# Kernel tuning notes

Measured on AMD Instinct MI355X. Metric: run time of the kernel, lower is better.

## Reference

```python
import jax, jax.numpy as jnp
import numpy as np

CODEBOOK_SIZE = 4096
DIM = 64


def setup_inputs() -> dict:
    key = jax.random.key(0)
    kx, ke = jax.random.split(key)
    x = jax.random.normal(kx, (8, 4096, DIM), dtype=jnp.float32)
    embed = jax.random.normal(ke, (CODEBOOK_SIZE, DIM), dtype=jnp.float32)  # codebook [K, d]
    return {"x": x, "embed": embed}


def reference(x, embed):
    # Eval-mode forward of EuclideanCodebook (svq_temp=None -> argmax).
    shape = x.shape
    flatten = x.reshape(-1, shape[-1])            # [N, d]
    embed_sq = jnp.sum(embed * embed, axis=-1)    # [K]
    # dist = 2 * x @ embed.T - ||embed||^2  (negative squared distance up to a const in x)
    dist = 2.0 * jnp.matmul(flatten, embed.T) - embed_sq[None, :]  # [N, K]
    embed_ind = jnp.argmax(dist, axis=-1)         # [N]
    embed_ind = embed_ind.reshape(shape[:-1])     # [...]
    quantize = embed[embed_ind]                   # gather -> [..., d]
    return (quantize, embed_ind)
```

## Files before the change

kernel.cpp:

```cpp
#include <hip/hip_runtime.h>
#include <math.h>

#define N_ROWS 32768
#define K_CODES 4096
#define DIM 64
#define SPLITS 4
#define TILES_TOTAL (K_CODES / 32)
#define TILES_PER_SPLIT (TILES_TOTAL / SPLITS)
#define QUANT_ELEMS (N_ROWS * DIM)

typedef _Float16 half8 __attribute__((ext_vector_type(8)));
typedef float floatx16 __attribute__((ext_vector_type(16)));

__device__ __forceinline__ void gld16(const void* g, void* l) {
    __builtin_amdgcn_global_load_lds(
        (const __attribute__((address_space(1))) unsigned int*)g,
        (__attribute__((address_space(3))) unsigned int*)l, 16, 0, 0);
}

__global__ void prep_kernel(const float* __restrict__ embed,
                            float* __restrict__ sq, half8* __restrict__ ehi,
                            half8* __restrict__ elo) {
    __shared__ float part[256];
    const int tid = threadIdx.x;
    const int t = blockIdx.x * 256 + tid;
    const int l = t & 63;
    const int s = (t >> 6) & 3;
    const int c = blockIdx.x;
    const int col = l & 31;
    const int code = c * 32 + col;
    const int koff = (l >> 5) * 8 + 16 * s;
    const float* src = embed + (size_t)code * DIM + koff;
    half8 h, lo;
    float ss = 0.f;
#pragma unroll
    for (int j = 0; j < 8; ++j) {
        float v = src[j];
        ss = fmaf(v, v, ss);
        _Float16 hi = (_Float16)v;
        h[j] = hi;
        lo[j] = (_Float16)(v - (float)hi);
    }
    ehi[t] = h;
    elo[t] = lo;
    part[tid] = ss;
    __syncthreads();
    if (tid < 32) {
        float a = 0.f;
#pragma unroll
        for (int q = 0; q < 8; ++q) a += part[tid + 32 * (q & 1) + 64 * (q >> 1)];
        sq[c * 32 + tid] = a;
    }
}

__global__ __launch_bounds__(256, 4) void fused_dist_argmax32(
    const float* __restrict__ x, const float* __restrict__ sq,
    const half8* __restrict__ ehi, const half8* __restrict__ elo,
    float* __restrict__ pbest, int* __restrict__ pidx) {
    __shared__ char lbuf[8192];
    const int tid = threadIdx.x;
    const int lane = tid & 63;
    const int wave = tid >> 6;
    const int col = lane & 31;
    const int half_ = lane >> 5;
    const int row_base = blockIdx.x * 128 + wave * 32;
    const int split = blockIdx.y;
    const int c0 = split * TILES_PER_SPLIT;

    half8 ah[4], al[4];
    {
        const float* xs = x + (size_t)(row_base + col) * DIM + half_ * 8;
#pragma unroll
        for (int s = 0; s < 4; ++s) {
            half8 h, lo;
#pragma unroll
            for (int j = 0; j < 8; ++j) {
                float v = 2.0f * xs[16 * s + j];
                _Float16 hi = (_Float16)v;
                h[j] = hi;
                lo[j] = (_Float16)(v - (float)hi);
            }
            ah[s] = h;
            al[s] = lo;
        }
    }

    float best[16];
    int bidx[16];
#pragma unroll
    for (int r = 0; r < 16; ++r) {
        best[r] = -INFINITY;
        bidx[r] = 0;
    }

    const char* gh = (const char*)(ehi + (size_t)c0 * 256);
    const char* gl = (const char*)(elo + (size_t)c0 * 256);
    const float* psq = sq + c0 * 32 + col;
    const half8* lh = (const half8*)lbuf;
    const half8* ll = (const half8*)(lbuf + 4096);

    for (int c = 0; c < TILES_PER_SPLIT; ++c) {
        gld16(gh + (size_t)c * 4096 + (size_t)tid * 16, lbuf + tid * 16);
        gld16(gl + (size_t)c * 4096 + (size_t)tid * 16, lbuf + 4096 + tid * 16);
        float nsq = -psq[(size_t)c * 32];
        __syncthreads();

        floatx16 acc;
#pragma unroll
        for (int r = 0; r < 16; ++r) acc[r] = nsq;
        half8 b;
        b = lh[lane];
        acc = __builtin_amdgcn_mfma_f32_32x32x16_f16(ah[0], b, acc, 0, 0, 0);
        acc = __builtin_amdgcn_mfma_f32_32x32x16_f16(al[0], b, acc, 0, 0, 0);
        b = lh[64 + lane];
        acc = __builtin_amdgcn_mfma_f32_32x32x16_f16(ah[1], b, acc, 0, 0, 0);
        acc = __builtin_amdgcn_mfma_f32_32x32x16_f16(al[1], b, acc, 0, 0, 0);
        b = lh[128 + lane];
        acc = __builtin_amdgcn_mfma_f32_32x32x16_f16(ah[2], b, acc, 0, 0, 0);
        acc = __builtin_amdgcn_mfma_f32_32x32x16_f16(al[2], b, acc, 0, 0, 0);
        b = lh[192 + lane];
        acc = __builtin_amdgcn_mfma_f32_32x32x16_f16(ah[3], b, acc, 0, 0, 0);
        acc = __builtin_amdgcn_mfma_f32_32x32x16_f16(al[3], b, acc, 0, 0, 0);
        b = ll[lane];
        acc = __builtin_amdgcn_mfma_f32_32x32x16_f16(ah[0], b, acc, 0, 0, 0);
        b = ll[64 + lane];
        acc = __builtin_amdgcn_mfma_f32_32x32x16_f16(ah[1], b, acc, 0, 0, 0);
        b = ll[128 + lane];
        acc = __builtin_amdgcn_mfma_f32_32x32x16_f16(ah[2], b, acc, 0, 0, 0);
        b = ll[192 + lane];
        acc = __builtin_amdgcn_mfma_f32_32x32x16_f16(ah[3], b, acc, 0, 0, 0);
        __syncthreads();

        const int cidx = (c0 + c) * 32 + col;
#pragma unroll
        for (int r = 0; r < 16; ++r) {
            if (acc[r] > best[r]) {
                best[r] = acc[r];
                bidx[r] = cidx;
            }
        }
    }

#pragma unroll
    for (int r = 0; r < 16; ++r) {
        float bv = best[r];
        int bi = bidx[r];
#pragma unroll
        for (int d = 1; d < 32; d <<= 1) {
            float ov = __shfl_xor(bv, d);
            int oi = __shfl_xor(bi, d);
            if (ov > bv || (ov == bv && oi < bi)) {
                bv = ov;
                bi = oi;
            }
        }
        if (col == 0) {
            const int row = row_base + (r & 3) + 8 * (r >> 2) + 4 * half_;
            pbest[(size_t)split * N_ROWS + row] = bv;
            pidx[(size_t)split * N_ROWS + row] = bi;
        }
    }
}

__global__ void combine_kernel(const float* __restrict__ pbest,
                               const int* __restrict__ pidx,
                               const float* __restrict__ embed,
                               float* __restrict__ out) {
    const int t = blockIdx.x * blockDim.x + threadIdx.x;
    const int row = t >> 4;
    const int q = t & 15;
    if (row >= N_ROWS) return;

    float best = -INFINITY;
    int bi = 0;
#pragma unroll
    for (int s = 0; s < SPLITS; ++s) {
        float b = pbest[(size_t)s * N_ROWS + row];
        int i = pidx[(size_t)s * N_ROWS + row];
        if (b > best) {
            best = b;
            bi = i;
        }
    }

    const float4* e4 = reinterpret_cast<const float4*>(embed);
    float4 v = e4[(size_t)bi * (DIM / 4) + q];
    reinterpret_cast<float4*>(out)[(size_t)row * (DIM / 4) + q] = v;
    if (q == 0) {
        out[(size_t)QUANT_ELEMS + row] = (float)bi;
    }
}

extern "C" void kernel_launch(void* const* d_in, const int* in_sizes, int n_in,
                              void* d_out, int out_size, void* d_ws,
                              size_t ws_size, hipStream_t stream) {
    const float* x = (const float*)d_in[0];
    const float* embed = (const float*)d_in[1];
    float* out = (float*)d_out;

    char* ws = (char*)d_ws;
    float* sq = (float*)ws;
    half8* ehi = (half8*)(ws + 16384);
    half8* elo = (half8*)(ws + 16384 + 524288);
    float* pbest = (float*)(ws + 16384 + 2 * 524288);
    int* pidx = (int*)(ws + 16384 + 2 * 524288 + SPLITS * N_ROWS * 4);

    prep_kernel<<<TILES_TOTAL, 256, 0, stream>>>(embed, sq, ehi, elo);

    dim3 grid(N_ROWS / 128, SPLITS);
    fused_dist_argmax32<<<grid, 256, 0, stream>>>(x, sq, ehi, elo, pbest,
                                                  pidx);

    const int combine_threads = N_ROWS * (DIM / 4);
    combine_kernel<<<(combine_threads + 255) / 256, 256, 0, stream>>>(
        pbest, pidx, embed, out);
}
```

Measured before the change: 120.8 us.

## Double-buffer codebook tiles in LDS with prefetch and MFMA priority

The main distance/argmax loop now loads two 32-code tiles per phase into one of two LDS buffers while computing on the other. Each iteration issues the next phase's global-to-LDS loads first, runs both subtiles, then waits on vmcnt and a single barrier. This replaces the two barriers per tile and the exposed load latency. It also raises wave priority around the MFMA chains, and doubles LDS to 32KB per block, which may limit occupancy.

```diff
diff --git a/kernel.cpp b/kernel.cpp
--- a/kernel.cpp
+++ b/kernel.cpp
@@ -7,6 +7,7 @@
 #define SPLITS 4
 #define TILES_TOTAL (K_CODES / 32)
 #define TILES_PER_SPLIT (TILES_TOTAL / SPLITS)
+#define PHASES (TILES_PER_SPLIT / 2)
 #define QUANT_ELEMS (N_ROWS * DIM)
 
 typedef _Float16 half8 __attribute__((ext_vector_type(8)));
@@ -53,11 +54,49 @@
     }
 }
 
+#define SUBTILE(LH, LL, NSQ, CIDX)                                            \
+    {                                                                         \
+        const half8* lh = (const half8*)(LH);                                 \
+        const half8* ll = (const half8*)(LL);                                 \
+        floatx16 acc;                                                         \
+        _Pragma("unroll") for (int r = 0; r < 16; ++r) acc[r] = (NSQ);        \
+        half8 b;                                                              \
+        __builtin_amdgcn_s_setprio(1);                                        \
+        b = lh[lane];                                                         \
+        acc = __builtin_amdgcn_mfma_f32_32x32x16_f16(ah[0], b, acc, 0, 0, 0); \
+        acc = __builtin_amdgcn_mfma_f32_32x32x16_f16(al[0], b, acc, 0, 0, 0); \
+        b = lh[64 + lane];                                                    \
+        acc = __builtin_amdgcn_mfma_f32_32x32x16_f16(ah[1], b, acc, 0, 0, 0); \
+        acc = __builtin_amdgcn_mfma_f32_32x32x16_f16(al[1], b, acc, 0, 0, 0); \
+        b = lh[128 + lane];                                                   \
+        acc = __builtin_amdgcn_mfma_f32_32x32x16_f16(ah[2], b, acc, 0, 0, 0); \
+        acc = __builtin_amdgcn_mfma_f32_32x32x16_f16(al[2], b, acc, 0, 0, 0); \
+        b = lh[192 + lane];                                                   \
+        acc = __builtin_amdgcn_mfma_f32_32x32x16_f16(ah[3], b, acc, 0, 0, 0); \
+        acc = __builtin_amdgcn_mfma_f32_32x32x16_f16(al[3], b, acc, 0, 0, 0); \
+        b = ll[lane];                                                         \
+        acc = __builtin_amdgcn_mfma_f32_32x32x16_f16(ah[0], b, acc, 0, 0, 0); \
+        b = ll[64 + lane];                                                    \
+        acc = __builtin_amdgcn_mfma_f32_32x32x16_f16(ah[1], b, acc, 0, 0, 0); \
+        b = ll[128 + lane];                                                   \
+        acc = __builtin_amdgcn_mfma_f32_32x32x16_f16(ah[2], b, acc, 0, 0, 0); \
+        b = ll[192 + lane];                                                   \
+        acc = __builtin_amdgcn_mfma_f32_32x32x16_f16(ah[3], b, acc, 0, 0, 0); \
+        __builtin_amdgcn_s_setprio(0);                                        \
+        const int cidx = (CIDX);                                              \
+        _Pragma("unroll") for (int r = 0; r < 16; ++r) {                      \
+            if (acc[r] > best[r]) {    \
+                best[r] = acc[r];                                             \
+                bidx[r] = cidx;                                               \
+            }                                                                 \
+        }                                                                     \
+    }
+
 __global__ __launch_bounds__(256, 4) void fused_dist_argmax32(
     const float* __restrict__ x, const float* __restrict__ sq,
     const half8* __restrict__ ehi, const half8* __restrict__ elo,
     float* __restrict__ pbest, int* __restrict__ pidx) {
-    __shared__ char lbuf[8192];
+    __shared__ __align__(16) char lbuf[2][16384];
     const int tid = threadIdx.x;
     const int lane = tid & 63;
     const int wave = tid >> 6;
@@ -96,49 +135,42 @@
     const char* gh = (const char*)(ehi + (size_t)c0 * 256);
     const char* gl = (const char*)(elo + (size_t)c0 * 256);
     const float* psq = sq + c0 * 32 + col;
-    const half8* lh = (const half8*)lbuf;
-    const half8* ll = (const half8*)(lbuf + 4096);
-
-    for (int c = 0; c < TILES_PER_SPLIT; ++c) {
-        gld16(gh + (size_t)c * 4096 + (size_t)tid * 16, lbuf + tid * 16);
-        gld16(gl + (size_t)c * 4096 + (size_t)tid * 16, lbuf + 4096 + tid * 16);
-        float nsq = -psq[(size_t)c * 32];
-        __syncthreads();
-
-        floatx16 acc;
-#pragma unroll
-        for (int r = 0; r < 16; ++r) acc[r] = nsq;
-        half8 b;
-        b = lh[lane];
-        acc = __builtin_amdgcn_mfma_f32_32x32x16_f16(ah[0], b, acc, 0, 0, 0);
-        acc = __builtin_amdgcn_mfma_f32_32x32x16_f16(al[0], b, acc, 0, 0, 0);
-        b = lh[64 + lane];
-        acc = __builtin_amdgcn_mfma_f32_32x32x16_f16(ah[1], b, acc, 0, 0, 0);
-        acc = __builtin_amdgcn_mfma_f32_32x32x16_f16(al[1], b, acc, 0, 0, 0);
-        b = lh[128 + lane];
-        acc = __builtin_amdgcn_mfma_f32_32x32x16_f16(ah[2], b, acc, 0, 0, 0);
-        acc = __builtin_amdgcn_mfma_f32_32x32x16_f16(al[2], b, acc, 0, 0, 0);
-        b = lh[192 + lane];
-        acc = __builtin_amdgcn_mfma_f32_32x32x16_f16(ah[3], b, acc, 0, 0, 0);
-        acc = __builtin_amdgcn_mfma_f32_32x32x16_f16(al[3], b, acc, 0, 0, 0);
-        b = ll[lane];
-        acc = __builtin_amdgcn_mfma_f32_32x32x16_f16(ah[0], b, acc, 0, 0, 0);
-        b = ll[64 + lane];
-        acc = __builtin_amdgcn_mfma_f32_32x32x16_f16(ah[1], b, acc, 0, 0, 0);
-        b = ll[128 + lane];
-        acc = __builtin_amdgcn_mfma_f32_32x32x16_f16(ah[2], b, acc, 0, 0, 0);
-        b = ll[192 + lane];
-        acc = __builtin_amdgcn_mfma_f32_32x32x16_f16(ah[3], b, acc, 0, 0, 0);
-        __syncthreads();
-
-        const int cidx = (c0 + c) * 32 + col;
-#pragma unroll
-        for (int r = 0; r < 16; ++r) {
-            if (acc[r] > best[r]) {
-                best[r] = acc[r];
-                bidx[r] = cidx;
-            }
-        }
+
+    {
+        char* d = lbuf[0];
+        gld16(gh + (size_t)tid * 16, d + tid * 16);
+        gld16(gl + (size_t)tid * 16, d + 4096 + tid * 16);
+        gld16(gh + 4096 + (size_t)tid * 16, d + 8192 + tid * 16);
+        gld16(gl + 4096 + (size_t)tid * 16, d + 12288 + tid * 16);
+    }
+    float nsqA = -psq[0];
+    float nsqB = -psq[32];
+    asm volatile("s_waitcnt vmcnt(0)" ::: "memory");
+    __builtin_amdgcn_s_barrier();
+    asm volatile("" ::: "memory");
+
+    for (int p = 0; p < PHASES; ++p) {
+        char* bufc = lbuf[p & 1];
+        if (p + 1 < PHASES) {
+            char* bufn = lbuf[(p & 1) ^ 1];
+            const size_t go = (size_t)(2 * p + 2) * 4096;
+            gld16(gh + go + (size_t)tid * 16, bufn + tid * 16);
+            gld16(gl + go + (size_t)tid * 16, bufn + 4096 + tid * 16);
+            gld16(gh + go + 4096 + (size_t)tid * 16, bufn + 8192 + tid * 16);
+            gld16(gl + go + 4096 + (size_t)tid * 16, bufn + 12288 + tid * 16);
+        }
+        const float nsq0 = nsqA, nsq1 = nsqB;
+        if (p + 1 < PHASES) {
+            nsqA = -psq[(2 * p + 2) * 32];
+            nsqB = -psq[(2 * p + 3) * 32];
+        }
+
+        SUBTILE(bufc, bufc + 4096, nsq0, (c0 + 2 * p) * 32 + col);
+        SUBTILE(bufc + 8192, bufc + 12288, nsq1, (c0 + 2 * p + 1) * 32 + col);
+
+        asm volatile("s_waitcnt vmcnt(0)" ::: "memory");
+        __builtin_amdgcn_s_barrier();
+        asm volatile("" ::: "memory");
     }
 
 #pragma unroll
```

Measured after the change: 123.3 us. 2.1% more time.

## Load codebook tiles directly to registers and software-pipeline argmax behind MFMA

Applied to the files above, without the earlier changes.

The LDS staging buffer and both per-tile barriers are dropped, so each wave now loads the hi/lo codebook fragments straight from global memory into registers. The argmax compare for the previous tile is deferred into the next iteration so it can overlap with the current tile's MFMA chain, and s_setprio raises wave priority around the MFMA block. The aim is to remove barrier stalls and LDS round trips. In exchange, each of the four waves in a block now fetches the same tile from global/L2 separately (four times the global traffic), and an extra 16-register accumulator is kept live.

```diff
diff --git a/kernel.cpp b/kernel.cpp
--- a/kernel.cpp
+++ b/kernel.cpp
@@ -11,12 +11,6 @@
 
 typedef _Float16 half8 __attribute__((ext_vector_type(8)));
 typedef float floatx16 __attribute__((ext_vector_type(16)));
-
-__device__ __forceinline__ void gld16(const void* g, void* l) {
-    __builtin_amdgcn_global_load_lds(
-        (const __attribute__((address_space(1))) unsigned int*)g,
-        (__attribute__((address_space(3))) unsigned int*)l, 16, 0, 0);
-}
 
 __global__ void prep_kernel(const float* __restrict__ embed,
                             float* __restrict__ sq, half8* __restrict__ ehi,
@@ -53,11 +47,10 @@
     }
 }
 
-__global__ __launch_bounds__(256, 4) void fused_dist_argmax32(
+__global__ __launch_bounds__(256, 4) void fused_dist_argmax_g(
     const float* __restrict__ x, const float* __restrict__ sq,
     const half8* __restrict__ ehi, const half8* __restrict__ elo,
     float* __restrict__ pbest, int* __restrict__ pidx) {
-    __shared__ char lbuf[8192];
     const int tid = threadIdx.x;
     const int lane = tid & 63;
     const int wave = tid >> 6;
@@ -93,51 +86,67 @@
         bidx[r] = 0;
     }
 
-    const char* gh = (const char*)(ehi + (size_t)c0 * 256);
-    const char* gl = (const char*)(elo + (size_t)c0 * 256);
+    const half8* gh = ehi + (size_t)c0 * 256;
+    const half8* gl = elo + (size_t)c0 * 256;
     const float* psq = sq + c0 * 32 + col;
-    const half8* lh = (const half8*)lbuf;
-    const half8* ll = (const half8*)(lbuf + 4096);
-
+
+    floatx16 accP;
+    int cidxP = 0;
+    bool haveP = false;
+
+#pragma unroll 1
     for (int c = 0; c < TILES_PER_SPLIT; ++c) {
-        gld16(gh + (size_t)c * 4096 + (size_t)tid * 16, lbuf + tid * 16);
-        gld16(gl + (size_t)c * 4096 + (size_t)tid * 16, lbuf + 4096 + tid * 16);
-        float nsq = -psq[(size_t)c * 32];
-        __syncthreads();
+        const half8* th = gh + (size_t)c * 256;
+        const half8* tl = gl + (size_t)c * 256;
+        half8 b0 = th[lane];
+        half8 b1 = th[64 + lane];
+        half8 b2 = th[128 + lane];
+        half8 b3 = th[192 + lane];
+        half8 l0 = tl[lane];
+        half8 l1 = tl[64 + lane];
+        half8 l2 = tl[128 + lane];
+        half8 l3 = tl[192 + lane];
+        const float nsq = -psq[(size_t)c * 32];
+
+        if (haveP) {
+#pragma unroll
+            for (int r = 0; r < 16; ++r) {
+                if (accP[r] > best[r]) {
+                    best[r] = accP[r];
+                    bidx[r] = cidxP;
+                }
+            }
+        }
 
         floatx16 acc;
 #pragma unroll
         for (int r = 0; r < 16; ++r) acc[r] = nsq;
-        half8 b;
-        b = lh[lane];
-        acc = __builtin_amdgcn_mfma_f32_32x32x16_f16(ah[0], b, acc, 0, 0, 0);
-        acc = __builtin_amdgcn_mfma_f32_32x32x16_f16(al[0], b, acc, 0, 0, 0);
-        b = lh[64 + lane];
-        acc = __builtin_amdgcn_mfma_f32_32x32x16_f16(ah[1], b, acc, 0, 0, 0);
-        acc = __builtin_amdgcn_mfma_f32_32x32x16_f16(al[1], b, acc, 0, 0, 0);
-        b = lh[128 + lane];
-        acc = __builtin_amdgcn_mfma_f32_32x32x16_f16(ah[2], b, acc, 0, 0, 0);
-        acc = __builtin_amdgcn_mfma_f32_32x32x16_f16(al[2], b, acc, 0, 0, 0);
-        b = lh[192 + lane];
-        acc = __builtin_amdgcn_mfma_f32_32x32x16_f16(ah[3], b, acc, 0, 0, 0);
-        acc = __builtin_amdgcn_mfma_f32_32x32x16_f16(al[3], b, acc, 0, 0, 0);
-        b = ll[lane];
-        acc = __builtin_amdgcn_mfma_f32_32x32x16_f16(ah[0], b, acc, 0, 0, 0);
-        b = ll[64 + lane];
-        acc = __builtin_amdgcn_mfma_f32_32x32x16_f16(ah[1], b, acc, 0, 0, 0);
-        b = ll[128 + lane];
-        acc = __builtin_amdgcn_mfma_f32_32x32x16_f16(ah[2], b, acc, 0, 0, 0);
-        b = ll[192 + lane];
-        acc = __builtin_amdgcn_mfma_f32_32x32x16_f16(ah[3], b, acc, 0, 0, 0);
-        __syncthreads();
-
-        const int cidx = (c0 + c) * 32 + col;
-#pragma unroll
-        for (int r = 0; r < 16; ++r) {
-            if (acc[r] > best[r]) {
-                best[r] = acc[r];
-                bidx[r] = cidx;
-            }
+
+        __builtin_amdgcn_s_setprio(1);
+        acc = __builtin_amdgcn_mfma_f32_32x32x16_f16(ah[0], b0, acc, 0, 0, 0);
+        acc = __builtin_amdgcn_mfma_f32_32x32x16_f16(al[0], b0, acc, 0, 0, 0);
+        acc = __builtin_amdgcn_mfma_f32_32x32x16_f16(ah[1], b1, acc, 0, 0, 0);
+        acc = __builtin_amdgcn_mfma_f32_32x32x16_f16(al[1], b1, acc, 0, 0, 0);
+        acc = __builtin_amdgcn_mfma_f32_32x32x16_f16(ah[2], b2, acc, 0, 0, 0);
+        acc = __builtin_amdgcn_mfma_f32_32x32x16_f16(al[2], b2, acc, 0, 0, 0);
+        acc = __builtin_amdgcn_mfma_f32_32x32x16_f16(ah[3], b3, acc, 0, 0, 0);
+        acc = __builtin_amdgcn_mfma_f32_32x32x16_f16(al[3], b3, acc, 0, 0, 0);
+        acc = __builtin_amdgcn_mfma_f32_32x32x16_f16(ah[0], l0, acc, 0, 0, 0);
+        acc = __builtin_amdgcn_mfma_f32_32x32x16_f16(ah[1], l1, acc, 0, 0, 0);
+        acc = __builtin_amdgcn_mfma_f32_32x32x16_f16(ah[2], l2, acc, 0, 0, 0);
+        acc = __builtin_amdgcn_mfma_f32_32x32x16_f16(ah[3], l3, acc, 0, 0, 0);
+        __builtin_amdgcn_s_setprio(0);
+
+        accP = acc;
+        cidxP = (c0 + c) * 32 + col;
+        haveP = true;
+    }
+
+#pragma unroll
+    for (int r = 0; r < 16; ++r) {
+        if (accP[r] > best[r]) {
+            best[r] = accP[r];
+            bidx[r] = cidxP;
         }
     }
 
@@ -208,7 +217,7 @@
     prep_kernel<<<TILES_TOTAL, 256, 0, stream>>>(embed, sq, ehi, elo);
 
     dim3 grid(N_ROWS / 128, SPLITS);
-    fused_dist_argmax32<<<grid, 256, 0, stream>>>(x, sq, ehi, elo, pbest,
+    fused_dist_argmax_g<<<grid, 256, 0, stream>>>(x, sq, ehi, elo, pbest,
                                                   pidx);
 
     const int combine_threads = N_ROWS * (DIM / 4);
```

Measured after the change: 136.7 us. 1.13x slower.

## Multi-stage LDS prefetch pipeline and atomic packed-key argmax combine

Applied to the files above, without the earlier changes.

Replaces the single-buffer load/sync/compute loop with a 4-slot LDS ring that prefetches three codebook tiles ahead, using explicit vmcnt waits and one barrier per tile. Caches the split's squared norms in LDS and raises wave priority around the MFMA chain. The per-split partial best values are replaced by a 64-bit packed (ordered float, inverted index) key merged with atomicMax, which simplifies the combine kernel. The larger LDS footprint could limit occupancy, and the ordering relies on the hand-written waitcnt counts.

```diff
diff --git a/kernel.cpp b/kernel.cpp
--- a/kernel.cpp
+++ b/kernel.cpp
@@ -20,10 +20,12 @@
 
 __global__ void prep_kernel(const float* __restrict__ embed,
                             float* __restrict__ sq, half8* __restrict__ ehi,
-                            half8* __restrict__ elo) {
+                            half8* __restrict__ elo,
+                            unsigned long long* __restrict__ keys) {
     __shared__ float part[256];
     const int tid = threadIdx.x;
     const int t = blockIdx.x * 256 + tid;
+    keys[t] = 0ull;
     const int l = t & 63;
     const int s = (t >> 6) & 3;
     const int c = blockIdx.x;
@@ -56,8 +58,10 @@
 __global__ __launch_bounds__(256, 4) void fused_dist_argmax32(
     const float* __restrict__ x, const float* __restrict__ sq,
     const half8* __restrict__ ehi, const half8* __restrict__ elo,
-    float* __restrict__ pbest, int* __restrict__ pidx) {
-    __shared__ char lbuf[8192];
+    unsigned long long* __restrict__ keys) {
+    __shared__ __align__(16) char lbuf[4][8192];
+    __shared__ float sqs[TILES_PER_SPLIT * 32];
+
     const int tid = threadIdx.x;
     const int lane = tid & 63;
     const int wave = tid >> 6;
@@ -95,20 +99,46 @@
 
     const char* gh = (const char*)(ehi + (size_t)c0 * 256);
     const char* gl = (const char*)(elo + (size_t)c0 * 256);
-    const float* psq = sq + c0 * 32 + col;
-    const half8* lh = (const half8*)lbuf;
-    const half8* ll = (const half8*)(lbuf + 4096);
-
-    for (int c = 0; c < TILES_PER_SPLIT; ++c) {
-        gld16(gh + (size_t)c * 4096 + (size_t)tid * 16, lbuf + tid * 16);
-        gld16(gl + (size_t)c * 4096 + (size_t)tid * 16, lbuf + 4096 + tid * 16);
-        float nsq = -psq[(size_t)c * 32];
-        __syncthreads();
+
+    {
+        const float4 v = reinterpret_cast<const float4*>(sq + c0 * 32)[tid];
+        reinterpret_cast<float4*>(sqs)[tid] = v;
+    }
+#pragma unroll
+    for (int t = 0; t < 3; ++t) {
+        char* d = lbuf[t];
+        gld16(gh + (size_t)t * 4096 + (size_t)tid * 16, d + tid * 16);
+        gld16(gl + (size_t)t * 4096 + (size_t)tid * 16, d + 4096 + tid * 16);
+    }
+
+#pragma unroll
+    for (int t = 0; t < TILES_PER_SPLIT; ++t) {
+        if (t < TILES_PER_SPLIT - 2)
+            asm volatile("s_waitcnt vmcnt(4)" ::: "memory");
+        else if (t == TILES_PER_SPLIT - 2)
+            asm volatile("s_waitcnt vmcnt(2)" ::: "memory");
+        else
+            asm volatile("s_waitcnt vmcnt(0)" ::: "memory");
+        __builtin_amdgcn_s_barrier();
+        asm volatile("" ::: "memory");
+
+        if (t + 3 < TILES_PER_SPLIT) {
+            char* d = lbuf[(t + 3) & 3];
+            gld16(gh + (size_t)(t + 3) * 4096 + (size_t)tid * 16, d + tid * 16);
+            gld16(gl + (size_t)(t + 3) * 4096 + (size_t)tid * 16,
+                  d + 4096 + tid * 16);
+        }
+
+        const half8* lh = (const half8*)lbuf[t & 3];
+        const half8* ll = (const half8*)(lbuf[t & 3] + 4096);
+        const float nsqv = -sqs[t * 32 + col];
 
         floatx16 acc;
 #pragma unroll
-        for (int r = 0; r < 16; ++r) acc[r] = nsq;
+        for (int r = 0; r < 16; ++r) acc[r] = nsqv;
+
         half8 b;
+        __builtin_amdgcn_s_setprio(1);
         b = lh[lane];
         acc = __builtin_amdgcn_mfma_f32_32x32x16_f16(ah[0], b, acc, 0, 0, 0);
         acc = __builtin_amdgcn_mfma_f32_32x32x16_f16(al[0], b, acc, 0, 0, 0);
@@ -129,9 +159,9 @@
         acc = __builtin_amdgcn_mfma_f32_32x32x16_f16(ah[2], b, acc, 0, 0, 0);
         b = ll[192 + lane];
         acc = __builtin_amdgcn_mfma_f32_32x32x16_f16(ah[3], b, acc, 0, 0, 0);
-        __syncthreads();
-
-        const int cidx = (c0 + c) * 32 + col;
+        __builtin_amdgcn_s_setprio(0);
+
+        const int cidx = (c0 + t) * 32 + col;
 #pragma unroll
         for (int r = 0; r < 16; ++r) {
             if (acc[r] > best[r]) {
@@ -156,14 +186,16 @@
         }
         if (col == 0) {
             const int row = row_base + (r & 3) + 8 * (r >> 2) + 4 * half_;
-            pbest[(size_t)split * N_ROWS + row] = bv;
-            pidx[(size_t)split * N_ROWS + row] = bi;
-        }
-    }
-}
-
-__global__ void combine_kernel(const float* __restrict__ pbest,
-                               const int* __restrict__ pidx,
+            unsigned ub = __float_as_uint(bv);
+            unsigned mapped = ub ^ (((int)ub >> 31) | 0x80000000u);
+            unsigned long long key =
+                ((unsigned long long)mapped << 32) | (unsigned)(~bi);
+            atomicMax(keys + row, key);
+        }
+    }
+}
+
+__global__ void combine_kernel(const unsigned long long* __restrict__ keys,
                                const float* __restrict__ embed,
                                float* __restrict__ out) {
     const int t = blockIdx.x * blockDim.x + threadIdx.x;
@@ -171,17 +203,8 @@
     const int q = t & 15;
     if (row >= N_ROWS) return;
 
-    float best = -INFINITY;
-    int bi = 0;
-#pragma unroll
-    for (int s = 0; s < SPLITS; ++s) {
-        float b = pbest[(size_t)s * N_ROWS + row];
-        int i = pidx[(size_t)s * N_ROWS + row];
-        if (b > best) {
-            best = b;
-            bi = i;
-        }
-    }
+    const unsigned long long key = keys[row];
+    const int bi = (int)(~(unsigned)key);
 
     const float4* e4 = reinterpret_cast<const float4*>(embed);
     float4 v = e4[(size_t)bi * (DIM / 4) + q];
@@ -202,16 +225,15 @@
     float* sq = (float*)ws;
     half8* ehi = (half8*)(ws + 16384);
     half8* elo = (half8*)(ws + 16384 + 524288);
-    float* pbest = (float*)(ws + 16384 + 2 * 524288);
-    int* pidx = (int*)(ws + 16384 + 2 * 524288 + SPLITS * N_ROWS * 4);
-
-    prep_kernel<<<TILES_TOTAL, 256, 0, stream>>>(embed, sq, ehi, elo);
+    unsigned long long* keys =
+        (unsigned long long*)(ws + 16384 + 2 * 524288);
+
+    prep_kernel<<<TILES_TOTAL, 256, 0, stream>>>(embed, sq, ehi, elo, keys);
 
     dim3 grid(N_ROWS / 128, SPLITS);
-    fused_dist_argmax32<<<grid, 256, 0, stream>>>(x, sq, ehi, elo, pbest,
-                                                  pidx);
+    fused_dist_argmax32<<<grid, 256, 0, stream>>>(x, sq, ehi, elo, keys);
 
     const int combine_threads = N_ROWS * (DIM / 4);
     combine_kernel<<<(combine_threads + 255) / 256, 256, 0, stream>>>(
-        pbest, pidx, embed, out);
-}
+        keys, embed, out);
+}
```

After: 139.8 us. 1.16x slower.
